# Kernel tuning notes

Hardware: AMD Instinct MI355X
Metric: run time of the kernel (lower is better)

## Reference

```python
import jax, jax.numpy as jnp
import numpy as np

HIDDEN = 2048
NUM_HEADS = 16
HEAD_DIM = HIDDEN // NUM_HEADS
INIT_RANGE = 0.02


def setup_inputs() -> dict:
    key = jax.random.key(0)
    ks = jax.random.split(key, 5)
    B, S = 2, 2048
    hidden_states = jax.random.normal(ks[0], (B, S, HIDDEN), dtype=jnp.float32)
    # Linear weights stored torch-style [out, in]; biases zero-init per _init_weights
    def w(k):
        return INIT_RANGE * jax.random.normal(k, (HIDDEN, HIDDEN), dtype=jnp.float32)
    return {
        "hidden_states": hidden_states,
        "wq": w(ks[1]), "bq": jnp.zeros((HIDDEN,), jnp.float32),
        "wk": w(ks[2]), "bk": jnp.zeros((HIDDEN,), jnp.float32),
        "wv": w(ks[3]), "bv": jnp.zeros((HIDDEN,), jnp.float32),
        "wo": w(ks[4]), "bo": jnp.zeros((HIDDEN,), jnp.float32),
    }


def _split_heads(x):
    # [B,S,H] -> [B,nh,S,hd]
    B, S, _ = x.shape
    return x.reshape(B, S, NUM_HEADS, HEAD_DIM).transpose(0, 2, 1, 3)


def reference(hidden_states, wq, bq, wk, bk, wv, bv, wo, bo):
    B, S, H = hidden_states.shape
    scale = 1.0 / np.sqrt(HEAD_DIM).astype(np.float32)

    q = _split_heads(hidden_states @ wq.T + bq)  # [B,nh,S,hd]
    k = _split_heads(hidden_states @ wk.T + bk)
    v = _split_heads(hidden_states @ wv.T + bv)

    attn = jnp.einsum('bhqd,bhkd->bhqk', q, k) * scale  # [B,nh,S,S]
    # causal mask: -inf above diagonal, 0 on/below
    causal = jnp.where(
        jnp.tril(jnp.ones((S, S), dtype=bool)),
        jnp.float32(0.0), jnp.float32(-jnp.inf))
    attn = attn + causal
    probs = jax.nn.softmax(attn, axis=-1)
    out = jnp.einsum('bhqk,bhkd->bhqd', probs, v)  # [B,nh,S,hd]
    out = out.transpose(0, 2, 1, 3).reshape(B, S, H)  # merge heads
    return out @ wo.T + bo
```

## Files before the change

### kernel.cpp

```cpp
#include <hip/hip_runtime.h>
#include <stdint.h>

typedef unsigned short u16;
typedef __attribute__((ext_vector_type(8))) short short8;
typedef __attribute__((ext_vector_type(4))) short short4v;
typedef __attribute__((ext_vector_type(4))) float float4v;

union V8u { short8 v; short4v h[2]; u16 u[8]; unsigned w[4]; };

__device__ __forceinline__ u16 f2bf(float f) {
  unsigned u = __float_as_uint(f);
  u = u + 0x7FFFu + ((u >> 16) & 1u);
  return (u16)(u >> 16);
}
__device__ __forceinline__ float4v fzero() {
  float4v z = {0.f, 0.f, 0.f, 0.f};
  return z;
}
__device__ __forceinline__ void gl_lds16(const u16* g, u16* l) {
  __builtin_amdgcn_global_load_lds(
      (const __attribute__((address_space(1))) void*)g,
      (__attribute__((address_space(3))) void*)l, 16, 0, 0);
}

#define MFMA16(a, b, c) __builtin_amdgcn_mfma_f32_16x16x32_bf16((a), (b), (c), 0, 0, 0)

__global__ void conv5_f32_bf16(const float* __restrict__ X,
                               const float* __restrict__ w0,
                               const float* __restrict__ w1,
                               const float* __restrict__ w2,
                               u16* __restrict__ dst, long seg) {
  const int y = blockIdx.y;
  const float* s = (y < 2) ? (X + (long)y * seg)
                           : (y == 2 ? w0 : (y == 3 ? w1 : w2));
  u16* d = dst + (long)y * seg;
  const long i = ((long)blockIdx.x * 256 + threadIdx.x) * 8;
  if (i >= seg) return;
  float4 a = *(const float4*)&s[i];
  float4 b = *(const float4*)&s[i + 4];
  V8u o;
  o.u[0] = f2bf(a.x); o.u[1] = f2bf(a.y); o.u[2] = f2bf(a.z); o.u[3] = f2bf(a.w);
  o.u[4] = f2bf(b.x); o.u[5] = f2bf(b.y); o.u[6] = f2bf(b.z); o.u[7] = f2bf(b.w);
  *(short8*)&d[i] = o.v;
}

__global__ void conv_f32_bf16(const float* __restrict__ in, u16* __restrict__ out, long n) {
  const long i = ((long)blockIdx.x * 256 + threadIdx.x) * 8;
  if (i >= n) return;
  float4 a = *(const float4*)&in[i];
  float4 b = *(const float4*)&in[i + 4];
  V8u o;
  o.u[0] = f2bf(a.x); o.u[1] = f2bf(a.y); o.u[2] = f2bf(a.z); o.u[3] = f2bf(a.w);
  o.u[4] = f2bf(b.x); o.u[5] = f2bf(b.y); o.u[6] = f2bf(b.z); o.u[7] = f2bf(b.w);
  *(short8*)&out[i] = o.v;
}

template <bool OUTF32>
__global__ __launch_bounds__(256, 2) void gemm_bt_bias(
    const u16* __restrict__ X,
    const u16* __restrict__ W0, const float* __restrict__ B0, void* __restrict__ O0,
    const u16* __restrict__ W1, const float* __restrict__ B1, void* __restrict__ O1,
    const u16* __restrict__ W2, const float* __restrict__ B2, void* __restrict__ O2,
    int M, int N, int K)
{
  const u16* W = W0; const float* Bb = B0; void* Ov = O0;
  if (blockIdx.z == 1) { W = W1; Bb = B1; Ov = O1; }
  else if (blockIdx.z == 2) { W = W2; Bb = B2; Ov = O2; }

  __shared__ u16 As[128 * 32];
  __shared__ u16 Bs[128 * 32];

  const int t = threadIdx.x;
  const int lane = t & 63, wave = t >> 6;
  const int quad = lane >> 4, l16 = lane & 15;
  const int wm = wave >> 1, wn = wave & 1;
  const long m0 = (long)blockIdx.y * 128;
  const long n0 = (long)blockIdx.x * 128;

  const int srow = t >> 2;
  const int scol = (t & 3) * 8;

  float4v acc[4][4];
  #pragma unroll
  for (int i = 0; i < 4; ++i)
    #pragma unroll
    for (int j = 0; j < 4; ++j) acc[i][j] = fzero();

  for (int k0 = 0; k0 < K; k0 += 32) {
    gl_lds16(&X[(m0 + srow) * K + k0 + scol],      &As[t * 8]);
    gl_lds16(&X[(m0 + srow + 64) * K + k0 + scol], &As[t * 8 + 64 * 32]);
    gl_lds16(&W[(n0 + srow) * K + k0 + scol],      &Bs[t * 8]);
    gl_lds16(&W[(n0 + srow + 64) * K + k0 + scol], &Bs[t * 8 + 64 * 32]);
    __syncthreads();

    short8 a[4], b[4];
    #pragma unroll
    for (int mi = 0; mi < 4; ++mi)
      a[mi] = *(const short8*)&As[(wm * 64 + mi * 16 + l16) * 32 + quad * 8];
    #pragma unroll
    for (int ni = 0; ni < 4; ++ni)
      b[ni] = *(const short8*)&Bs[(wn * 64 + ni * 16 + l16) * 32 + quad * 8];
    #pragma unroll
    for (int mi = 0; mi < 4; ++mi)
      #pragma unroll
      for (int ni = 0; ni < 4; ++ni)
        acc[mi][ni] = MFMA16(a[mi], b[ni], acc[mi][ni]);
    __syncthreads();
  }

  #pragma unroll
  for (int ni = 0; ni < 4; ++ni) {
    const long cg = n0 + wn * 64 + ni * 16 + l16;
    const float bv = Bb[cg];
    #pragma unroll
    for (int mi = 0; mi < 4; ++mi) {
      const long rg0 = m0 + wm * 64 + mi * 16 + quad * 4;
      #pragma unroll
      for (int r = 0; r < 4; ++r) {
        const float v = acc[mi][ni][r] + bv;
        if (OUTF32) ((float*)Ov)[(rg0 + r) * N + cg] = v;
        else        ((u16*)Ov)[(rg0 + r) * N + cg] = f2bf(v);
      }
    }
  }
}

#define S_LEN 2048
#define HID   2048
#define HD    128

__global__ __launch_bounds__(256, 2) void attn_fwd(
    const u16* __restrict__ Q, const u16* __restrict__ K,
    const u16* __restrict__ V, u16* __restrict__ Ctx)
{
  __shared__ u16 Ks[2][32 * 136];
  __shared__ unsigned Vt[2][128 * 17];
  __shared__ u16 Ps[4 * 2 * 512];

  const int t = threadIdx.x;
  const int lane = t & 63, wave = t >> 6;
  const int quad = lane >> 4, l16 = lane & 15;
  const int qb = (int)(gridDim.x - 1 - blockIdx.x) * 128;
  const int b = blockIdx.y >> 4, h = blockIdx.y & 15;

  const long base = (long)b * S_LEN * HID + (long)h * HD;
  const u16* Qp = Q + base;
  const u16* Kp = K + base;
  const u16* Vp = V + base;

  const int sr2 = t >> 4;
  const int sc8 = (t & 15) * 8;
  const int wqb = qb + wave * 32;

  short8 qf[2][4];
  #pragma unroll
  for (int g = 0; g < 2; ++g) {
    const long qr = wqb + g * 16 + l16;
    #pragma unroll
    for (int kk = 0; kk < 4; ++kk)
      qf[g][kk] = *(const short8*)&Qp[qr * HID + kk * 32 + quad * 8];
  }

  short8 onesv;
  {
    V8u ou;
    #pragma unroll
    for (int j = 0; j < 8; ++j) ou.u[j] = 0x3F80;
    onesv = ou.v;
  }

  float4v o[2][9];
  #pragma unroll
  for (int g = 0; g < 2; ++g)
    #pragma unroll
    for (int i = 0; i < 9; ++i) o[g][i] = fzero();
  const float SC = 0.08838834764831845f * 1.4426950408889634f;

  short8 kr0, kr1, vv0, vv1;
  {
    const long g = (long)(2 * sr2) * HID + sc8;
    kr0 = *(const short8*)&Kp[g];
    kr1 = *(const short8*)&Kp[g + HID];
    vv0 = *(const short8*)&Vp[g];
    vv1 = *(const short8*)&Vp[g + HID];
  }
  {
    *(short8*)&Ks[0][(2 * sr2) * 136 + sc8]     = kr0;
    *(short8*)&Ks[0][(2 * sr2 + 1) * 136 + sc8] = kr1;
    V8u a, c; a.v = vv0; c.v = vv1;
    #pragma unroll
    for (int j = 0; j < 8; ++j)
      Vt[0][(sc8 + j) * 17 + sr2] = (unsigned)a.u[j] | ((unsigned)c.u[j] << 16);
  }
  __syncthreads();

  const int T = (qb + 128) >> 5;
  for (int ti = 0; ti < T; ++ti) {
    const int kv0 = ti << 5;
    const int p = ti & 1;

    const bool more = (ti + 1 < T);
    if (more) {
      const long g = (long)(kv0 + 32 + 2 * sr2) * HID + sc8;
      kr0 = *(const short8*)&Kp[g];
      kr1 = *(const short8*)&Kp[g + HID];
      vv0 = *(const short8*)&Vp[g];
      vv1 = *(const short8*)&Vp[g + HID];
    }

    if (kv0 <= wqb) {
      float4v s[2][2];
      #pragma unroll
      for (int g = 0; g < 2; ++g) { s[g][0] = fzero(); s[g][1] = fzero(); }
      #pragma unroll
      for (int ni = 0; ni < 2; ++ni)
        #pragma unroll
        for (int kk = 0; kk < 4; ++kk) {
          short8 kf = *(const short8*)&Ks[p][(ni * 16 + l16) * 136 + kk * 32 + quad * 8];
          s[0][ni] = MFMA16(qf[0][kk], kf, s[0][ni]);
          s[1][ni] = MFMA16(qf[1][kk], kf, s[1][ni]);
        }

      const int pb = wave * 1024;
      #pragma unroll
      for (int g = 0; g < 2; ++g) {
        const int qrow0 = wqb + g * 16 + quad * 4;
        #pragma unroll
        for (int r = 0; r < 4; ++r) {
          float s0 = fminf(s[g][0][r] * SC, 80.f);
          float s1 = fminf(s[g][1][r] * SC, 80.f);
          if (kv0 + l16 > qrow0 + r)      s0 = -1e30f;
          if (kv0 + 16 + l16 > qrow0 + r) s1 = -1e30f;
          Ps[pb + g * 512 + (quad * 4 + r) * 32 + l16]      = f2bf(__builtin_amdgcn_exp2f(s0));
          Ps[pb + g * 512 + (quad * 4 + r) * 32 + 16 + l16] = f2bf(__builtin_amdgcn_exp2f(s1));
        }
      }
      __threadfence_block();
      short8 pf0 = *(const short8*)&Ps[pb + l16 * 32 + quad * 8];
      short8 pf1 = *(const short8*)&Ps[pb + 512 + l16 * 32 + quad * 8];

      #pragma unroll
      for (int dt = 0; dt < 8; ++dt) {
        const unsigned* vp = &Vt[p][(dt * 16 + l16) * 17 + quad * 4];
        V8u vf;
        vf.w[0] = vp[0]; vf.w[1] = vp[1]; vf.w[2] = vp[2]; vf.w[3] = vp[3];
        o[0][dt] = MFMA16(pf0, vf.v, o[0][dt]);
        o[1][dt] = MFMA16(pf1, vf.v, o[1][dt]);
      }
      o[0][8] = MFMA16(pf0, onesv, o[0][8]);
      o[1][8] = MFMA16(pf1, onesv, o[1][8]);
    }

    if (more) {
      *(short8*)&Ks[1 - p][(2 * sr2) * 136 + sc8]     = kr0;
      *(short8*)&Ks[1 - p][(2 * sr2 + 1) * 136 + sc8] = kr1;
      V8u a, c; a.v = vv0; c.v = vv1;
      #pragma unroll
      for (int j = 0; j < 8; ++j)
        Vt[1 - p][(sc8 + j) * 17 + sr2] = (unsigned)a.u[j] | ((unsigned)c.u[j] << 16);
    }
    __syncthreads();
  }

  u16* Cp = Ctx + base;
  #pragma unroll
  for (int g = 0; g < 2; ++g)
    #pragma unroll
    for (int r = 0; r < 4; ++r) {
      const float inv = 1.0f / o[g][8][r];
      const long qr = wqb + g * 16 + quad * 4 + r;
      #pragma unroll
      for (int dt = 0; dt < 8; ++dt)
        Cp[qr * HID + dt * 16 + l16] = f2bf(o[g][dt][r] * inv);
    }
}

extern "C" void kernel_launch(void* const* d_in, const int* in_sizes, int n_in,
                              void* d_out, int out_size, void* d_ws, size_t ws_size,
                              hipStream_t stream) {
  const float* X  = (const float*)d_in[0];
  const float* wq = (const float*)d_in[1];
  const float* bq = (const float*)d_in[2];
  const float* wk = (const float*)d_in[3];
  const float* bk = (const float*)d_in[4];
  const float* wv = (const float*)d_in[5];
  const float* bv = (const float*)d_in[6];
  const float* wo = (const float*)d_in[7];
  const float* bo = (const float*)d_in[8];
  float* out = (float*)d_out;

  const long HSZ = 4096L * 2048;
  const long WSZ = 2048L * 2048;
  u16* Qw = (u16*)d_ws;
  u16* Kw = Qw + HSZ;
  u16* Vw = Kw + HSZ;
  u16* Xb = Vw + HSZ;
  u16* Wb = Xb + HSZ;
  u16* W0 = Wb, *W1 = Wb + WSZ, *W2 = Wb + 2 * WSZ;

  dim3 blk(256);
  conv5_f32_bf16<<<dim3((int)(WSZ / 2048), 5), blk, 0, stream>>>(X, wq, wk, wv, Xb, WSZ);

  gemm_bt_bias<false><<<dim3(16, 32, 3), blk, 0, stream>>>(
      Xb, W0, bq, Qw, W1, bk, Kw, W2, bv, Vw, 4096, 2048, 2048);

  attn_fwd<<<dim3(16, 32), blk, 0, stream>>>(Qw, Kw, Vw, Qw);

  conv_f32_bf16<<<(int)(WSZ / 2048), blk, 0, stream>>>(wo, W0, WSZ);
  gemm_bt_bias<true><<<dim3(16, 32, 1), blk, 0, stream>>>(
      Qw, W0, bo, out, W0, bo, out, W0, bo, out, 4096, 2048, 2048);
}
```

Measured before the change: 441.0 us.

## Use 256x256-tile fused QKV GEMM with 4-stage direct-to-LDS pipeline

Replaces the 128x128-tile, three-z-slice QKV projection with a single 512-thread kernel using 256x256 output tiles over the concatenated Wq/Wk/Wv matrix. Global data is loaded straight into swizzled LDS through a 4-deep ring buffer, and wave priority is raised around the MFMA block. The goal is more reuse per loaded byte and better hiding of memory latency. In exchange it uses much more LDS and many more accumulator registers, so occupancy drops, and the grid has only 384 blocks.

Result: slower. 450.7 us (+2.2%).

```diff
diff --git a/kernel.cpp b/kernel.cpp
--- a/kernel.cpp
+++ b/kernel.cpp
@@ -55,6 +55,117 @@
   *(short8*)&out[i] = o.v;
 }
 
+__global__ __launch_bounds__(512, 2) void gemm256_qkv(
+    const u16* __restrict__ X, const u16* __restrict__ Wb,
+    const float* __restrict__ bq, const float* __restrict__ bk,
+    const float* __restrict__ bv, u16* __restrict__ Out, int K)
+{
+  __shared__ u16 AB[4][2][8192];
+
+  const int t = threadIdx.x;
+  const int lane = t & 63;
+  const int wave = t >> 6;
+  const int quad = lane >> 4, l16 = lane & 15;
+  const int wm = wave >> 2, wn = wave & 3;
+
+  const long m0 = (long)blockIdx.y * 256;
+  const long n0 = (long)blockIdx.x * 256;
+
+  int arow[2], acol[2];
+  #pragma unroll
+  for (int l = 0; l < 2; ++l) {
+    const int o = l * 8192 + t * 16;
+    const int lg = o ^ ((o >> 3) & 0x30);
+    arow[l] = lg >> 6;
+    acol[l] = (lg & 63) >> 1;
+  }
+  const u16* bAs[2]; const u16* bBs[2];
+  #pragma unroll
+  for (int l = 0; l < 2; ++l) {
+    bAs[l] = X  + (m0 + arow[l]) * K + acol[l];
+    bBs[l] = Wb + (n0 + arow[l]) * K + acol[l];
+  }
+  const int dA0 = t * 8, dA1 = 4096 + t * 8;
+
+  int offA[8], offB[4];
+  #pragma unroll
+  for (int i = 0; i < 8; ++i) {
+    const int r = wm * 128 + i * 16 + l16;
+    const int lg = r * 64 + quad * 16;
+    offA[i] = (lg ^ ((lg >> 3) & 0x30)) >> 1;
+  }
+  #pragma unroll
+  for (int n = 0; n < 4; ++n) {
+    const int r = wn * 64 + n * 16 + l16;
+    const int lg = r * 64 + quad * 16;
+    offB[n] = (lg ^ ((lg >> 3) & 0x30)) >> 1;
+  }
+
+  float4v acc[8][4];
+  #pragma unroll
+  for (int i = 0; i < 8; ++i)
+    #pragma unroll
+    for (int n = 0; n < 4; ++n) acc[i][n] = fzero();
+
+  #pragma unroll
+  for (int c = 0; c < 3; ++c) {
+    u16* Ad = &AB[c][0][0];
+    u16* Bd = &AB[c][1][0];
+    gl_lds16(bAs[0] + c * 32, Ad + dA0);
+    gl_lds16(bBs[0] + c * 32, Bd + dA0);
+    gl_lds16(bAs[1] + c * 32, Ad + dA1);
+    gl_lds16(bBs[1] + c * 32, Bd + dA1);
+  }
+  asm volatile("s_waitcnt vmcnt(8)\n\ts_barrier" ::: "memory");
+
+  const int NCH = K >> 5;
+  for (int c = 0; c < NCH; ++c) {
+    const u16* Ac = &AB[c & 3][0][0];
+    const u16* Bc = &AB[c & 3][1][0];
+
+    short8 b[4], a[8];
+    #pragma unroll
+    for (int n = 0; n < 4; ++n) b[n] = *(const short8*)&Bc[offB[n]];
+    #pragma unroll
+    for (int i = 0; i < 8; ++i) a[i] = *(const short8*)&Ac[offA[i]];
+
+    int cs = c + 3; if (cs >= NCH) cs = NCH - 1;
+    u16* Ad = &AB[(c + 3) & 3][0][0];
+    u16* Bd = &AB[(c + 3) & 3][1][0];
+    gl_lds16(bAs[0] + cs * 32, Ad + dA0);
+    gl_lds16(bBs[0] + cs * 32, Bd + dA0);
+    gl_lds16(bAs[1] + cs * 32, Ad + dA1);
+    gl_lds16(bBs[1] + cs * 32, Bd + dA1);
+    __builtin_amdgcn_sched_barrier(0);
+
+    __builtin_amdgcn_s_setprio(1);
+    #pragma unroll
+    for (int i = 0; i < 8; ++i)
+      #pragma unroll
+      for (int n = 0; n < 4; ++n)
+        acc[i][n] = MFMA16(a[i], b[n], acc[i][n]);
+    __builtin_amdgcn_s_setprio(0);
+
+    asm volatile("s_waitcnt vmcnt(8)\n\ts_barrier" ::: "memory");
+  }
+
+  #pragma unroll
+  for (int n = 0; n < 4; ++n) {
+    const int cg = (int)n0 + wn * 64 + n * 16 + l16;
+    const int z = cg >> 11, col = cg & 2047;
+    const float* Bp = (z == 0) ? bq : (z == 1 ? bk : bv);
+    const float bvv = Bp[col];
+    u16* Op = Out + (long)z * (4096L * 2048);
+    #pragma unroll
+    for (int i = 0; i < 8; ++i) {
+      const long r0 = m0 + wm * 128 + i * 16 + quad * 4;
+      #pragma unroll
+      for (int r = 0; r < 4; ++r)
+        Op[(r0 + r) * 2048 + col] = f2bf(acc[i][n][r] + bvv);
+    }
+  }
+}
+
 template <bool OUTF32>
 __global__ __launch_bounds__(256, 2) void gemm_bt_bias(
     const u16* __restrict__ X,
@@ -296,13 +407,13 @@
   u16* Vw = Kw + HSZ;
   u16* Xb = Vw + HSZ;
   u16* Wb = Xb + HSZ;
-  u16* W0 = Wb, *W1 = Wb + WSZ, *W2 = Wb + 2 * WSZ;
+  u16* W0 = Wb;
 
   dim3 blk(256);
   conv5_f32_bf16<<<dim3((int)(WSZ / 2048), 5), blk, 0, stream>>>(X, wq, wk, wv, Xb, WSZ);
 
-  gemm_bt_bias<false><<<dim3(16, 32, 3), blk, 0, stream>>>(
-      Xb, W0, bq, Qw, W1, bk, Kw, W2, bv, Vw, 4096, 2048, 2048);
+  gemm256_qkv<<<dim3(24, 16), dim3(512), 0, stream>>>(
+      Xb, Wb, bq, bk, bv, Qw, 2048);
 
   attn_fwd<<<dim3(16, 32), blk, 0, stream>>>(Qw, Kw, Vw, Qw);
 
```

## Replace QKV projection with 256x256-tile pipelined GEMM kernel

Applied to the files above, without the earlier changes.

Adds a new QKV projection GEMM that uses 256x256 output tiles with 512 threads, a double-buffered LDS pipeline fed by global_load_lds, XOR-swizzled LDS layout, and a block-index swizzle for L2 locality. It treats the three weight matrices as one contiguous N=6144 matrix and routes columns to Q/K/V when storing. The aim is more data reuse per tile and better overlap of loads with MFMA work than the previous 128-tile kernel. In exchange it uses larger LDS and register footprint, fewer resident blocks, and relies on hand-placed barriers and waitcnts.

New measurement: 435.7 us. No clear change (-1.2%).

```diff
diff --git a/kernel.cpp b/kernel.cpp
--- a/kernel.cpp
+++ b/kernel.cpp
@@ -55,6 +55,171 @@
   *(short8*)&out[i] = o.v;
 }
 
+__global__ __launch_bounds__(512, 2) void gemm256_qkv(
+    const u16* __restrict__ X, const u16* __restrict__ Wb,
+    const float* __restrict__ bq, const float* __restrict__ bk,
+    const float* __restrict__ bv, u16* __restrict__ Out, int K)
+{
+  __shared__ __align__(16) u16 lds[2][2][2][8192];
+
+  const int t = threadIdx.x;
+  const int lane = t & 63;
+  const int wave = t >> 6;
+  const int quad = lane >> 4, l16 = lane & 15;
+  const int wm = wave >> 2, wn = wave & 3;
+
+  const int bid = (int)blockIdx.x;
+  const int swz = (bid & 7) * 48 + (bid >> 3);
+  const int bx = swz >> 4;
+  const int by = swz & 15;
+  const long m0 = (long)by * 256;
+  const long n0 = (long)bx * 256;
+
+  const u16* pA[2]; const u16* pB[2];
+  #pragma unroll
+  for (int l = 0; l < 2; ++l) {
+    const int d = l * 8192 + t * 16;
+    const int o = d ^ ((d >> 3) & 0x70);
+    const int r = o >> 7;
+    const int c = (o & 127) >> 1;
+    pA[l] = X  + (m0 + r) * (long)K + c;
+    pB[l] = Wb + (n0 + r) * (long)K + c;
+  }
+
+  int offk[2];
+  #pragma unroll
+  for (int kk = 0; kk < 2; ++kk)
+    offk[kk] = l16 * 128 + ((kk * 64 + quad * 16) ^ ((l16 & 7) << 4));
+
+  float4v acc[8][4];
+  #pragma unroll
+  for (int i = 0; i < 8; ++i)
+    #pragma unroll
+    for (int n = 0; n < 4; ++n) acc[i][n] = fzero();
+
+#define STAGE(buf_, mat_, h_, kt_) do {                                        \
+    const long ko_ = (long)(h_) * 128 * K + (long)(kt_) * 64;                  \
+    gl_lds16(((mat_) ? pB[0] : pA[0]) + ko_, &lds[buf_][mat_][h_][t * 8]);     \
+    gl_lds16(((mat_) ? pB[1] : pA[1]) + ko_, &lds[buf_][mat_][h_][4096 + t * 8]); \
+  } while (0)
+
+#define BAR() do { asm volatile("s_barrier" ::: "memory");                     \
+                   __builtin_amdgcn_sched_barrier(0); } while (0)
+
+  const int NT = K >> 6;
+
+  STAGE(0, 0, 0, 0);
+  STAGE(0, 1, 0, 0);
+  STAGE(0, 0, 1, 0);
+  STAGE(0, 1, 1, 0);
+  STAGE(1, 0, 0, (NT > 1) ? 1 : 0);
+  asm volatile("s_waitcnt vmcnt(2)" ::: "memory");
+  BAR();
+
+  for (int kt = 0; kt < NT; ++kt) {
+    const int buf = kt & 1, nb = buf ^ 1;
+    const int kc1 = (kt + 1 < NT) ? kt + 1 : NT - 1;
+    const int kc2 = (kt + 2 < NT) ? kt + 2 : NT - 1;
+    const char* Ab = (const char*)&lds[buf][0][wm][0];
+    const char* Bb = (const char*)&lds[buf][1][wn >> 1][0] + (wn & 1) * 8192;
+
+    short8 a[4][2], b0[2][2], b1[2][2];
+
+    STAGE(nb, 1, 0, kc1);
+    #pragma unroll
+    for (int i = 0; i < 4; ++i)
+      #pragma unroll
+      for (int kk = 0; kk < 2; ++kk)
+        a[i][kk] = *(const short8*)(Ab + i * 2048 + offk[kk]);
+    #pragma unroll
+    for (int n = 0; n < 2; ++n)
+      #pragma unroll
+      for (int kk = 0; kk < 2; ++kk)
+        b0[n][kk] = *(const short8*)(Bb + n * 2048 + offk[kk]);
+    BAR();
+    __builtin_amdgcn_s_setprio(1);
+    #pragma unroll
+    for (int i = 0; i < 4; ++i)
+      #pragma unroll
+      for (int n = 0; n < 2; ++n)
+        #pragma unroll
+        for (int kk = 0; kk < 2; ++kk)
+          acc[i][n] = MFMA16(a[i][kk], b0[n][kk], acc[i][n]);
+    __builtin_amdgcn_s_setprio(0);
+    BAR();
+
+    STAGE(nb, 0, 1, kc1);
+    #pragma unroll
+    for (int n = 0; n < 2; ++n)
+      #pragma unroll
+      for (int kk = 0; kk < 2; ++kk)
+        b1[n][kk] = *(const short8*)(Bb + (2 + n) * 2048 + offk[kk]);
+    BAR();
+    __builtin_amdgcn_s_setprio(1);
+    #pragma unroll
+    for (int i = 0; i < 4; ++i)
+      #pragma unroll
+      for (int n = 0; n < 2; ++n)
+        #pragma unroll
+        for (int kk = 0; kk < 2; ++kk)
+          acc[i][2 + n] = MFMA16(a[i][kk], b1[n][kk], acc[i][2 + n]);
+    __builtin_amdgcn_s_setprio(0);
+    BAR();
+
+    STAGE(nb, 1, 1, kc1);
+    #pragma unroll
+    for (int i = 0; i < 4; ++i)
+      #pragma unroll
+      for (int kk = 0; kk < 2; ++kk)
+        a[i][kk] = *(const short8*)(Ab + 8192 + i * 2048 + offk[kk]);
+    BAR();
+    __builtin_amdgcn_s_setprio(1);
+    #pragma unroll
+    for (int i = 0; i < 4; ++i)
+      #pragma unroll
+      for (int n = 0; n < 2; ++n)
+        #pragma unroll
+        for (int kk = 0; kk < 2; ++kk)
+          acc[4 + i][2 + n] = MFMA16(a[i][kk], b1[n][kk], acc[4 + i][2 + n]);
+    __builtin_amdgcn_s_setprio(0);
+    BAR();
+
+    STAGE(buf, 0, 0, kc2);
+    asm volatile("s_waitcnt vmcnt(2)" ::: "memory");
+    BAR();
+    __builtin_amdgcn_s_setprio(1);
+    #pragma unroll
+    for (int i = 0; i < 4; ++i)
+      #pragma unroll
+      for (int n = 0; n < 2; ++n)
+        #pragma unroll
+        for (int kk = 0; kk < 2; ++kk)
+          acc[4 + i][n] = MFMA16(a[i][kk], b0[n][kk], acc[4 + i][n]);
+    __builtin_amdgcn_s_setprio(0);
+    BAR();
+  }
+  asm volatile("s_waitcnt vmcnt(0)" ::: "memory");
+
+#undef STAGE
+#undef BAR
+
+  #pragma unroll
+  for (int n = 0; n < 4; ++n) {
+    const int cg = (int)n0 + wn * 64 + n * 16 + l16;
+    const int z = cg >> 11, col = cg & 2047;
+    const float* Bp = (z == 0) ? bq : (z == 1 ? bk : bv);
+    const float bvv = Bp[col];
+    u16* Op = Out + (long)z * (4096L * 2048);
+    #pragma unroll
+    for (int i = 0; i < 8; ++i) {
+      const long r0 = m0 + wm * 128 + i * 16 + quad * 4;
+      #pragma unroll
+      for (int r = 0; r < 4; ++r)
+        Op[(r0 + r) * 2048 + col] = f2bf(acc[i][n][r] + bvv);
+    }
+  }
+}
+
 template <bool OUTF32>
 __global__ __launch_bounds__(256, 2) void gemm_bt_bias(
     const u16* __restrict__ X,
@@ -296,13 +461,13 @@
   u16* Vw = Kw + HSZ;
   u16* Xb = Vw + HSZ;
   u16* Wb = Xb + HSZ;
-  u16* W0 = Wb, *W1 = Wb + WSZ, *W2 = Wb + 2 * WSZ;
+  u16* W0 = Wb;
 
   dim3 blk(256);
   conv5_f32_bf16<<<dim3((int)(WSZ / 2048), 5), blk, 0, stream>>>(X, wq, wk, wv, Xb, WSZ);
 
-  gemm_bt_bias<false><<<dim3(16, 32, 3), blk, 0, stream>>>(
-      Xb, W0, bq, Qw, W1, bk, Kw, W2, bv, Vw, 4096, 2048, 2048);
+  gemm256_qkv<<<dim3(384), dim3(512), 0, stream>>>(
+      Xb, Wb, bq, bk, bv, Qw, 2048);
 
   attn_fwd<<<dim3(16, 32), blk, 0, stream>>>(Qw, Kw, Vw, Qw);
 
```

## Rewrite projection GEMM with triple-buffered 128x256 tiles and pair causal attention blocks

Applied to the files above, without the earlier changes.

Replaces the 128x128, single-stage GEMM with a 512-thread kernel. It uses 128x256 tiles and K=64 steps, triple-buffered async global-to-LDS loads, XOR-swizzled LDS layout, split MFMA phases with setprio, and a block-index swizzle for cache locality. The QKV projection now runs as one fused N=6144 GEMM over the contiguous converted weights. The attention kernel has each block handle two query tiles (x and 15-x) so causal work is balanced across blocks with half the grid. The large LDS footprint limits occupancy to one block per CU, and the hand-written waitcnt and barrier scheduling is fragile.

After: 394.0 us. 10.7% less time.

```diff
diff --git a/kernel.cpp b/kernel.cpp
--- a/kernel.cpp
+++ b/kernel.cpp
@@ -56,70 +56,138 @@
 }
 
 template <bool OUTF32>
-__global__ __launch_bounds__(256, 2) void gemm_bt_bias(
-    const u16* __restrict__ X,
-    const u16* __restrict__ W0, const float* __restrict__ B0, void* __restrict__ O0,
-    const u16* __restrict__ W1, const float* __restrict__ B1, void* __restrict__ O1,
-    const u16* __restrict__ W2, const float* __restrict__ B2, void* __restrict__ O2,
-    int M, int N, int K)
+__global__ __launch_bounds__(512, 2) void gemm_bal(
+    const u16* __restrict__ X, const u16* __restrict__ Wb,
+    const float* __restrict__ b0, const float* __restrict__ b1,
+    const float* __restrict__ b2, void* __restrict__ Out,
+    int K, int cpx)
 {
-  const u16* W = W0; const float* Bb = B0; void* Ov = O0;
-  if (blockIdx.z == 1) { W = W1; Bb = B1; Ov = O1; }
-  else if (blockIdx.z == 2) { W = W2; Bb = B2; Ov = O2; }
-
-  __shared__ u16 As[128 * 32];
-  __shared__ u16 Bs[128 * 32];
+  __shared__ __align__(16) u16 lds[3][3][8192];
 
   const int t = threadIdx.x;
-  const int lane = t & 63, wave = t >> 6;
+  const int lane = t & 63;
+  const int wave = t >> 6;
   const int quad = lane >> 4, l16 = lane & 15;
-  const int wm = wave >> 1, wn = wave & 1;
-  const long m0 = (long)blockIdx.y * 128;
-  const long n0 = (long)blockIdx.x * 128;
-
-  const int srow = t >> 2;
-  const int scol = (t & 3) * 8;
+  const int wm = wave >> 2, wn = wave & 3;
+
+  const int bid = (int)blockIdx.x;
+  const int swz = (bid & 7) * cpx + (bid >> 3);
+  const int by = swz & 31;
+  const int bx = swz >> 5;
+  const long m0 = (long)by * 128;
+  const long n0 = (long)bx * 256;
+
+  const u16* pA[2]; const u16* pBl[2]; const u16* pBu[2];
+  #pragma unroll
+  for (int l = 0; l < 2; ++l) {
+    const int d = l * 8192 + t * 16;
+    const int o = d ^ ((d >> 3) & 0x70);
+    const int r = o >> 7;
+    const int c = (o & 127) >> 1;
+    pA[l]  = X  + (m0 + r) * (long)K + c;
+    pBl[l] = Wb + (n0 + r) * (long)K + c;
+    pBu[l] = Wb + (n0 + 128 + r) * (long)K + c;
+  }
+
+  int offk[2];
+  #pragma unroll
+  for (int kk = 0; kk < 2; ++kk)
+    offk[kk] = l16 * 128 + ((kk * 64 + quad * 16) ^ ((l16 & 7) << 4));
 
   float4v acc[4][4];
   #pragma unroll
   for (int i = 0; i < 4; ++i)
     #pragma unroll
-    for (int j = 0; j < 4; ++j) acc[i][j] = fzero();
-
-  for (int k0 = 0; k0 < K; k0 += 32) {
-    gl_lds16(&X[(m0 + srow) * K + k0 + scol],      &As[t * 8]);
-    gl_lds16(&X[(m0 + srow + 64) * K + k0 + scol], &As[t * 8 + 64 * 32]);
-    gl_lds16(&W[(n0 + srow) * K + k0 + scol],      &Bs[t * 8]);
-    gl_lds16(&W[(n0 + srow + 64) * K + k0 + scol], &Bs[t * 8 + 64 * 32]);
-    __syncthreads();
-
-    short8 a[4], b[4];
-    #pragma unroll
-    for (int mi = 0; mi < 4; ++mi)
-      a[mi] = *(const short8*)&As[(wm * 64 + mi * 16 + l16) * 32 + quad * 8];
-    #pragma unroll
-    for (int ni = 0; ni < 4; ++ni)
-      b[ni] = *(const short8*)&Bs[(wn * 64 + ni * 16 + l16) * 32 + quad * 8];
-    #pragma unroll
-    for (int mi = 0; mi < 4; ++mi)
-      #pragma unroll
-      for (int ni = 0; ni < 4; ++ni)
-        acc[mi][ni] = MFMA16(a[mi], b[ni], acc[mi][ni]);
-    __syncthreads();
-  }
+    for (int n = 0; n < 4; ++n) acc[i][n] = fzero();
+
+#define STG(buf_, reg_, ptr_, kt_) do {                                        \
+    gl_lds16(ptr_[0] + (long)(kt_) * 64, &lds[buf_][reg_][t * 8]);             \
+    gl_lds16(ptr_[1] + (long)(kt_) * 64, &lds[buf_][reg_][4096 + t * 8]);      \
+  } while (0)
+
+#define BAR() do { asm volatile("s_barrier" ::: "memory");                     \
+                   __builtin_amdgcn_sched_barrier(0); } while (0)
+
+  const int NT = K >> 6;
+
+  STG(0, 0, pA, 0);  STG(0, 1, pBl, 0);  STG(0, 2, pBu, 0);
+  STG(1, 0, pA, 1);  STG(1, 1, pBl, 1);  STG(1, 2, pBu, 1);
+  asm volatile("s_waitcnt vmcnt(6)" ::: "memory");
+  BAR();
+
+  int buf = 0, sb = 2;
+  for (int kt = 0; kt < NT; ++kt) {
+    const int s2 = (kt + 2 < NT) ? kt + 2 : NT - 1;
+    const char* Ab = (const char*)&lds[buf][0][0] + wm * 8192;
+    const char* Bb = (const char*)&lds[buf][1 + (wn >> 1)][0] + (wn & 1) * 8192;
+
+    short8 a[4][2], b[4][2];
+
+    STG(sb, 0, pA, s2);
+    STG(sb, 1, pBl, s2);
+    #pragma unroll
+    for (int i = 0; i < 4; ++i)
+      #pragma unroll
+      for (int kk = 0; kk < 2; ++kk)
+        a[i][kk] = *(const short8*)(Ab + i * 2048 + offk[kk]);
+    #pragma unroll
+    for (int n = 0; n < 2; ++n)
+      #pragma unroll
+      for (int kk = 0; kk < 2; ++kk)
+        b[n][kk] = *(const short8*)(Bb + n * 2048 + offk[kk]);
+    BAR();
+    __builtin_amdgcn_s_setprio(1);
+    #pragma unroll
+    for (int i = 0; i < 4; ++i)
+      #pragma unroll
+      for (int n = 0; n < 2; ++n)
+        #pragma unroll
+        for (int kk = 0; kk < 2; ++kk)
+          acc[i][n] = MFMA16(a[i][kk], b[n][kk], acc[i][n]);
+    __builtin_amdgcn_s_setprio(0);
+    BAR();
+
+    STG(sb, 2, pBu, s2);
+    #pragma unroll
+    for (int n = 2; n < 4; ++n)
+      #pragma unroll
+      for (int kk = 0; kk < 2; ++kk)
+        b[n][kk] = *(const short8*)(Bb + n * 2048 + offk[kk]);
+    asm volatile("s_waitcnt vmcnt(6)" ::: "memory");
+    BAR();
+    __builtin_amdgcn_s_setprio(1);
+    #pragma unroll
+    for (int i = 0; i < 4; ++i)
+      #pragma unroll
+      for (int n = 2; n < 4; ++n)
+        #pragma unroll
+        for (int kk = 0; kk < 2; ++kk)
+          acc[i][n] = MFMA16(a[i][kk], b[n][kk], acc[i][n]);
+    __builtin_amdgcn_s_setprio(0);
+    BAR();
+
+    buf = (buf == 2) ? 0 : buf + 1;
+    sb  = (sb  == 2) ? 0 : sb  + 1;
+  }
+
+#undef STG
+#undef BAR
 
   #pragma unroll
-  for (int ni = 0; ni < 4; ++ni) {
-    const long cg = n0 + wn * 64 + ni * 16 + l16;
-    const float bv = Bb[cg];
-    #pragma unroll
-    for (int mi = 0; mi < 4; ++mi) {
-      const long rg0 = m0 + wm * 64 + mi * 16 + quad * 4;
+  for (int n = 0; n < 4; ++n) {
+    const int cg = (int)n0 + wn * 64 + n * 16 + l16;
+    const int z = cg >> 11, col = cg & 2047;
+    const float* Bp = (z == 0) ? b0 : (z == 1 ? b1 : b2);
+    const float bvv = Bp[col];
+    #pragma unroll
+    for (int i = 0; i < 4; ++i) {
+      const long r0 = m0 + wm * 64 + i * 16 + quad * 4;
       #pragma unroll
       for (int r = 0; r < 4; ++r) {
-        const float v = acc[mi][ni][r] + bv;
-        if (OUTF32) ((float*)Ov)[(rg0 + r) * N + cg] = v;
-        else        ((u16*)Ov)[(rg0 + r) * N + cg] = f2bf(v);
+        const long off = (long)z * (4096L * 2048) + (r0 + r) * 2048 + col;
+        const float v = acc[i][n][r] + bvv;
+        if (OUTF32) ((float*)Out)[off] = v;
+        else        ((u16*)Out)[off] = f2bf(v);
       }
     }
   }
@@ -140,26 +208,16 @@
   const int t = threadIdx.x;
   const int lane = t & 63, wave = t >> 6;
   const int quad = lane >> 4, l16 = lane & 15;
-  const int qb = (int)(gridDim.x - 1 - blockIdx.x) * 128;
   const int b = blockIdx.y >> 4, h = blockIdx.y & 15;
 
   const long base = (long)b * S_LEN * HID + (long)h * HD;
   const u16* Qp = Q + base;
   const u16* Kp = K + base;
   const u16* Vp = V + base;
+  u16* Cp = Ctx + base;
 
   const int sr2 = t >> 4;
   const int sc8 = (t & 15) * 8;
-  const int wqb = qb + wave * 32;
-
-  short8 qf[2][4];
-  #pragma unroll
-  for (int g = 0; g < 2; ++g) {
-    const long qr = wqb + g * 16 + l16;
-    #pragma unroll
-    for (int kk = 0; kk < 4; ++kk)
-      qf[g][kk] = *(const short8*)&Qp[qr * HID + kk * 32 + quad * 8];
-  }
 
   short8 onesv;
   {
@@ -168,111 +226,124 @@
     for (int j = 0; j < 8; ++j) ou.u[j] = 0x3F80;
     onesv = ou.v;
   }
-
-  float4v o[2][9];
-  #pragma unroll
-  for (int g = 0; g < 2; ++g)
-    #pragma unroll
-    for (int i = 0; i < 9; ++i) o[g][i] = fzero();
   const float SC = 0.08838834764831845f * 1.4426950408889634f;
 
-  short8 kr0, kr1, vv0, vv1;
-  {
-    const long g = (long)(2 * sr2) * HID + sc8;
-    kr0 = *(const short8*)&Kp[g];
-    kr1 = *(const short8*)&Kp[g + HID];
-    vv0 = *(const short8*)&Vp[g];
-    vv1 = *(const short8*)&Vp[g + HID];
-  }
-  {
-    *(short8*)&Ks[0][(2 * sr2) * 136 + sc8]     = kr0;
-    *(short8*)&Ks[0][(2 * sr2 + 1) * 136 + sc8] = kr1;
-    V8u a, c; a.v = vv0; c.v = vv1;
-    #pragma unroll
-    for (int j = 0; j < 8; ++j)
-      Vt[0][(sc8 + j) * 17 + sr2] = (unsigned)a.u[j] | ((unsigned)c.u[j] << 16);
-  }
-  __syncthreads();
-
-  const int T = (qb + 128) >> 5;
-  for (int ti = 0; ti < T; ++ti) {
-    const int kv0 = ti << 5;
-    const int p = ti & 1;
-
-    const bool more = (ti + 1 < T);
-    if (more) {
-      const long g = (long)(kv0 + 32 + 2 * sr2) * HID + sc8;
+  for (int pass = 0; pass < 2; ++pass) {
+    const int qb = (pass ? (int)blockIdx.x : 15 - (int)blockIdx.x) * 128;
+    const int wqb = qb + wave * 32;
+
+    short8 qf[2][4];
+    #pragma unroll
+    for (int g = 0; g < 2; ++g) {
+      const long qr = wqb + g * 16 + l16;
+      #pragma unroll
+      for (int kk = 0; kk < 4; ++kk)
+        qf[g][kk] = *(const short8*)&Qp[qr * HID + kk * 32 + quad * 8];
+    }
+
+    float4v o[2][9];
+    #pragma unroll
+    for (int g = 0; g < 2; ++g)
+      #pragma unroll
+      for (int i = 0; i < 9; ++i) o[g][i] = fzero();
+
+    short8 kr0, kr1, vv0, vv1;
+    {
+      const long g = (long)(2 * sr2) * HID + sc8;
       kr0 = *(const short8*)&Kp[g];
       kr1 = *(const short8*)&Kp[g + HID];
       vv0 = *(const short8*)&Vp[g];
       vv1 = *(const short8*)&Vp[g + HID];
     }
-
-    if (kv0 <= wqb) {
-      float4v s[2][2];
-      #pragma unroll
-      for (int g = 0; g < 2; ++g) { s[g][0] = fzero(); s[g][1] = fzero(); }
-      #pragma unroll
-      for (int ni = 0; ni < 2; ++ni)
-        #pragma unroll
-        for (int kk = 0; kk < 4; ++kk) {
-          short8 kf = *(const short8*)&Ks[p][(ni * 16 + l16) * 136 + kk * 32 + quad * 8];
-          s[0][ni] = MFMA16(qf[0][kk], kf, s[0][ni]);
-          s[1][ni] = MFMA16(qf[1][kk], kf, s[1][ni]);
+    {
+      *(short8*)&Ks[0][(2 * sr2) * 136 + sc8]     = kr0;
+      *(short8*)&Ks[0][(2 * sr2 + 1) * 136 + sc8] = kr1;
+      V8u a, c; a.v = vv0; c.v = vv1;
+      #pragma unroll
+      for (int j = 0; j < 8; ++j)
+        Vt[0][(sc8 + j) * 17 + sr2] = (unsigned)a.u[j] | ((unsigned)c.u[j] << 16);
+    }
+    __syncthreads();
+
+    const int T = (qb + 128) >> 5;
+    for (int ti = 0; ti < T; ++ti) {
+      const int kv0 = ti << 5;
+      const int p = ti & 1;
+
+      const bool more = (ti + 1 < T);
+      if (more) {
+        const long g = (long)(kv0 + 32 + 2 * sr2) * HID + sc8;
+        kr0 = *(const short8*)&Kp[g];
+        kr1 = *(const short8*)&Kp[g + HID];
+        vv0 = *(const short8*)&Vp[g];
+        vv1 = *(const short8*)&Vp[g + HID];
+      }
+
+      if (kv0 <= wqb) {
+        float4v s[2][2];
+        #pragma unroll
+        for (int g = 0; g < 2; ++g) { s[g][0] = fzero(); s[g][1] = fzero(); }
+        #pragma unroll
+        for (int ni = 0; ni < 2; ++ni)
+          #pragma unroll
+          for (int kk = 0; kk < 4; ++kk) {
+            short8 kf = *(const short8*)&Ks[p][(ni * 16 + l16) * 136 + kk * 32 + quad * 8];
+            s[0][ni] = MFMA16(qf[0][kk], kf, s[0][ni]);
+            s[1][ni] = MFMA16(qf[1][kk], kf, s[1][ni]);
+          }
+
+        const int pb = wave * 1024;
+        #pragma unroll
+        for (int g = 0; g < 2; ++g) {
+          const int qrow0 = wqb + g * 16 + quad * 4;
+          #pragma unroll
+          for (int r = 0; r < 4; ++r) {
+            float s0 = fminf(s[g][0][r] * SC, 80.f);
+            float s1 = fminf(s[g][1][r] * SC, 80.f);
+            if (kv0 + l16 > qrow0 + r)      s0 = -1e30f;
+            if (kv0 + 16 + l16 > qrow0 + r) s1 = -1e30f;
+            Ps[pb + g * 512 + (quad * 4 + r) * 32 + l16]      = f2bf(__builtin_amdgcn_exp2f(s0));
+            Ps[pb + g * 512 + (quad * 4 + r) * 32 + 16 + l16] = f2bf(__builtin_amdgcn_exp2f(s1));
+          }
         }
-
-      const int pb = wave * 1024;
-      #pragma unroll
-      for (int g = 0; g < 2; ++g) {
-        const int qrow0 = wqb + g * 16 + quad * 4;
-        #pragma unroll
-        for (int r = 0; r < 4; ++r) {
-          float s0 = fminf(s[g][0][r] * SC, 80.f);
-          float s1 = fminf(s[g][1][r] * SC, 80.f);
-          if (kv0 + l16 > qrow0 + r)      s0 = -1e30f;
-          if (kv0 + 16 + l16 > qrow0 + r) s1 = -1e30f;
-          Ps[pb + g * 512 + (quad * 4 + r) * 32 + l16]      = f2bf(__builtin_amdgcn_exp2f(s0));
-          Ps[pb + g * 512 + (quad * 4 + r) * 32 + 16 + l16] = f2bf(__builtin_amdgcn_exp2f(s1));
+        __threadfence_block();
+        short8 pf0 = *(const short8*)&Ps[pb + l16 * 32 + quad * 8];
+        short8 pf1 = *(const short8*)&Ps[pb + 512 + l16 * 32 + quad * 8];
+
+        #pragma unroll
+        for (int dt = 0; dt < 8; ++dt) {
+          const unsigned* vp = &Vt[p][(dt * 16 + l16) * 17 + quad * 4];
+          V8u vf;
+          vf.w[0] = vp[0]; vf.w[1] = vp[1]; vf.w[2] = vp[2]; vf.w[3] = vp[3];
+          o[0][dt] = MFMA16(pf0, vf.v, o[0][dt]);
+          o[1][dt] = MFMA16(pf1, vf.v, o[1][dt]);
         }
-      }
-      __threadfence_block();
-      short8 pf0 = *(const short8*)&Ps[pb + l16 * 32 + quad * 8];
-      short8 pf1 = *(const short8*)&Ps[pb + 512 + l16 * 32 + quad * 8];
-
-      #pragma unroll
-      for (int dt = 0; dt < 8; ++dt) {
-        const unsigned* vp = &Vt[p][(dt * 16 + l16) * 17 + quad * 4];
-        V8u vf;
-        vf.w[0] = vp[0]; vf.w[1] = vp[1]; vf.w[2] = vp[2]; vf.w[3] = vp[3];
-        o[0][dt] = MFMA16(pf0, vf.v, o[0][dt]);
-        o[1][dt] = MFMA16(pf1, vf.v, o[1][dt]);
-      }
-      o[0][8] = MFMA16(pf0, onesv, o[0][8]);
-      o[1][8] = MFMA16(pf1, onesv, o[1][8]);
-    }
-
-    if (more) {
-      *(short8*)&Ks[1 - p][(2 * sr2) * 136 + sc8]     = kr0;
-      *(short8*)&Ks[1 - p][(2 * sr2 + 1) * 136 + sc8] = kr1;
-      V8u a, c; a.v = vv0; c.v = vv1;
-      #pragma unroll
-      for (int j = 0; j < 8; ++j)
-        Vt[1 - p][(sc8 + j) * 17 + sr2] = (unsigned)a.u[j] | ((unsigned)c.u[j] << 16);
-    }
-    __syncthreads();
-  }
-
-  u16* Cp = Ctx + base;
-  #pragma unroll
-  for (int g = 0; g < 2; ++g)
-    #pragma unroll
-    for (int r = 0; r < 4; ++r) {
-      const float inv = 1.0f / o[g][8][r];
-      const long qr = wqb + g * 16 + quad * 4 + r;
-      #pragma unroll
-      for (int dt = 0; dt < 8; ++dt)
-        Cp[qr * HID + dt * 16 + l16] = f2bf(o[g][dt][r] * inv);
-    }
+        o[0][8] = MFMA16(pf0, onesv, o[0][8]);
+        o[1][8] = MFMA16(pf1, onesv, o[1][8]);
+      }
+
+      if (more) {
+        *(short8*)&Ks[1 - p][(2 * sr2) * 136 + sc8]     = kr0;
+        *(short8*)&Ks[1 - p][(2 * sr2 + 1) * 136 + sc8] = kr1;
+        V8u a, c; a.v = vv0; c.v = vv1;
+        #pragma unroll
+        for (int j = 0; j < 8; ++j)
+          Vt[1 - p][(sc8 + j) * 17 + sr2] = (unsigned)a.u[j] | ((unsigned)c.u[j] << 16);
+      }
+      __syncthreads();
+    }
+
+    #pragma unroll
+    for (int g = 0; g < 2; ++g)
+      #pragma unroll
+      for (int r = 0; r < 4; ++r) {
+        const float inv = 1.0f / o[g][8][r];
+        const long qr = wqb + g * 16 + quad * 4 + r;
+        #pragma unroll
+        for (int dt = 0; dt < 8; ++dt)
+          Cp[qr * HID + dt * 16 + l16] = f2bf(o[g][dt][r] * inv);
+      }
+  }
 }
 
 extern "C" void kernel_launch(void* const* d_in, const int* in_sizes, int n_in,
@@ -296,17 +367,17 @@
   u16* Vw = Kw + HSZ;
   u16* Xb = Vw + HSZ;
   u16* Wb = Xb + HSZ;
-  u16* W0 = Wb, *W1 = Wb + WSZ, *W2 = Wb + 2 * WSZ;
+  u16* W0 = Wb;
 
   dim3 blk(256);
   conv5_f32_bf16<<<dim3((int)(WSZ / 2048), 5), blk, 0, stream>>>(X, wq, wk, wv, Xb, WSZ);
 
-  gemm_bt_bias<false><<<dim3(16, 32, 3), blk, 0, stream>>>(
-      Xb, W0, bq, Qw, W1, bk, Kw, W2, bv, Vw, 4096, 2048, 2048);
-
-  attn_fwd<<<dim3(16, 32), blk, 0, stream>>>(Qw, Kw, Vw, Qw);
+  gemm_bal<false><<<dim3(768), dim3(512), 0, stream>>>(
+      Xb, Wb, bq, bk, bv, Qw, 2048, 96);
+
+  attn_fwd<<<dim3(8, 32), blk, 0, stream>>>(Qw, Kw, Vw, Qw);
 
   conv_f32_bf16<<<(int)(WSZ / 2048), blk, 0, stream>>>(wo, W0, WSZ);
-  gemm_bt_bias<true><<<dim3(16, 32, 1), blk, 0, stream>>>(
-      Qw, W0, bo, out, W0, bo, out, W0, bo, out, 4096, 2048, 2048);
-}
+  gemm_bal<true><<<dim3(256), dim3(512), 0, stream>>>(
+      Qw, W0, bo, bo, bo, out, 2048, 32);
+}
```
